# Performance work log

Measured on AMD Instinct MI355X. Metric: run time of the kernel, lower is better.

The kernel has to match this reference:

```python
import jax, jax.numpy as jnp
import numpy as np

N_HEAD = 16
SIZE_PER_HEAD = 64
NEG_BIG = 1e12


def _len_mask(lengths, T):
    # Faithful to: mask = 1 - cumsum(one_hot(len, T), 1)
    # -> 1.0 for positions < len, 0.0 for positions >= len (all ones if len == T).
    pos = jnp.arange(T)
    return (pos[None, :] < lengths[:, 0, None]).astype(jnp.float32)  # [B, T]


def setup_inputs() -> dict:
    key = jax.random.key(0)
    ks = jax.random.split(key, 8)
    B, T, D = 2, 2048, 1024
    Q_seq = jax.random.normal(ks[0], (B, T, D), dtype=jnp.float32)
    K_seq = jax.random.normal(ks[1], (B, T, D), dtype=jnp.float32)
    V_seq = jax.random.normal(ks[2], (B, T, D), dtype=jnp.float32)
    Q_len = jax.random.randint(ks[3], (B, 1), 0, T, dtype=jnp.int32)
    V_len = jax.random.randint(ks[4], (B, 1), 0, T, dtype=jnp.int32)
    s = 1.0 / np.sqrt(D)
    WQ = jax.random.normal(ks[5], (D, N_HEAD * SIZE_PER_HEAD), dtype=jnp.float32) * s
    WK = jax.random.normal(ks[6], (D, N_HEAD * SIZE_PER_HEAD), dtype=jnp.float32) * s
    WV = jax.random.normal(ks[7], (D, N_HEAD * SIZE_PER_HEAD), dtype=jnp.float32) * s
    return {"Q_seq": Q_seq, "K_seq": K_seq, "V_seq": V_seq,
            "Q_len": Q_len, "V_len": V_len, "WQ": WQ, "WK": WK, "WV": WV}


def reference(Q_seq, K_seq, V_seq, Q_len, V_len, WQ, WK, WV):
    B, Tq, _ = Q_seq.shape
    Tk = K_seq.shape[1]
    H, dh = N_HEAD, SIZE_PER_HEAD

    q = (Q_seq @ WQ).reshape(B, Tq, H, dh)  # [B,Tq,H,dh]
    k = (K_seq @ WK).reshape(B, Tk, H, dh)
    v = (V_seq @ WV).reshape(B, Tk, H, dh)

    # scaled dot-product scores [B,H,Tq,Tk]
    A = jnp.einsum('bqhd,bkhd->bhqk', q, k) / np.sqrt(dh).astype(np.float32)

    # additive key-length mask over the key axis (original: permute+mask+permute)
    kmask = _len_mask(V_len, Tk)  # [B,Tk]
    A = A - (1.0 - kmask)[:, None, None, :] * NEG_BIG
    A = jax.nn.softmax(A, axis=-1)

    O = jnp.einsum('bhqk,bkhd->bqhd', A, v).reshape(B, Tq, H * dh)

    # multiplicative query-length mask
    qmask = _len_mask(Q_len, Tq)  # [B,Tq]
    return O * qmask[:, :, None]
```

## Files before the change

### kernel.cpp

```cpp
#include <hip/hip_runtime.h>


using short8   = __attribute__((ext_vector_type(8))) short;
using floatx4  = __attribute__((ext_vector_type(4))) float;
using floatx16 = __attribute__((ext_vector_type(16))) float;
using uintx4   = __attribute__((ext_vector_type(4))) unsigned int;
using ushort4v = __attribute__((ext_vector_type(4))) unsigned short;

__device__ __forceinline__ unsigned short f2bf(float f) {
    unsigned int u = __builtin_bit_cast(unsigned int, f);
    u += 0x7fffu + ((u >> 16) & 1u);
    return (unsigned short)(u >> 16);
}

__global__ __launch_bounds__(256) void cvt_kernel(
    const float* __restrict__ Qs, const float* __restrict__ Ks,
    const float* __restrict__ Vs, const int* __restrict__ Qlen,
    const int* __restrict__ Vlen, unsigned short* __restrict__ abf)
{
    int z = blockIdx.y, row = blockIdx.x;
    int b = row >> 11, rib = row & 2047;
    int ql = Qlen[b]; int vl = Vlen[b]; int vle = vl ? vl : 2048;
    int lim = (z == 0) ? ((ql + 127) & ~127) : ((vle + 127) & ~127);
    if (rib >= lim) return;
    const float* src = (z == 0) ? Qs : ((z == 1) ? Ks : Vs);
    int t = threadIdx.x;
    float4 v = *reinterpret_cast<const float4*>(src + (size_t)row * 1024 + t * 4);
    ushort4v o;
    o[0] = f2bf(v.x); o[1] = f2bf(v.y); o[2] = f2bf(v.z); o[3] = f2bf(v.w);
    *reinterpret_cast<ushort4v*>(abf + (size_t)z * 4194304u + (size_t)row * 1024 + t * 4) = o;
}

__global__ __launch_bounds__(256) void wt_kernel(
    const float* __restrict__ W0, const float* __restrict__ W1,
    const float* __restrict__ W2, unsigned short* __restrict__ out)
{
    __shared__ float tile[64][65];
    int z = blockIdx.z;
    const float* W = (z == 0) ? W0 : ((z == 1) ? W1 : W2);
    unsigned short* O = out + (size_t)z * 1048576u;
    int r0 = blockIdx.y * 64, c0 = blockIdx.x * 64;
    int t = threadIdx.x;
#pragma unroll
    for (int i = 0; i < 16; i++) {
        int idx = t + i * 256; int r = idx >> 6, c = idx & 63;
        tile[r][c] = W[(size_t)(r0 + r) * 1024 + c0 + c];
    }
    __syncthreads();
#pragma unroll
    for (int i = 0; i < 16; i++) {
        int idx = t + i * 256; int c = idx >> 6, r = idx & 63;
        O[(size_t)(c0 + c) * 1024 + r0 + r] = f2bf(tile[r][c]);
    }
}

template <bool PRECVT>
__global__ __launch_bounds__(256) void proj_kernel(
    const float* __restrict__ Qs, const float* __restrict__ Ks,
    const float* __restrict__ Vs, const unsigned short* __restrict__ abf,
    const unsigned short* __restrict__ wt,
    const int* __restrict__ Qlen, const int* __restrict__ Vlen,
    unsigned short* __restrict__ q, unsigned short* __restrict__ k,
    unsigned short* __restrict__ vh)
{
    __shared__ alignas(16) unsigned short As[128][72];
    __shared__ alignas(16) unsigned short Bs[128][72];

    int z = blockIdx.z;
    int tid = threadIdx.x;
    int m0 = blockIdx.y * 128, n0 = blockIdx.x * 128;
    int b = m0 >> 11, rib = m0 & 2047;
    int ql = Qlen[b]; int vl = Vlen[b]; int vle = vl ? vl : 2048;
    int lim = (z == 0) ? ((ql + 127) & ~127) : ((vle + 127) & ~127);
    if (rib >= lim) return;

    const float* Af = (z == 0) ? Qs : ((z == 1) ? Ks : Vs);
    const unsigned short* Ab = abf + (size_t)z * 4194304u;
    const unsigned short* Bt = wt + (size_t)z * 1048576u;

    int w = tid >> 6, lane = tid & 63, g = lane >> 4, lr = lane & 15;
    int wr = w >> 1, wc = w & 1;

    floatx4 acc[4][4];
#pragma unroll
    for (int m = 0; m < 4; m++)
#pragma unroll
        for (int n = 0; n < 4; n++) {
#pragma unroll
            for (int r = 0; r < 4; r++) acc[m][n][r] = 0.f;
        }

    int srow = tid >> 1, scol = (tid & 1) * 32;

    short8 pa[4], pb[4];
    float4 fa[8];

    if constexpr (PRECVT) {
#pragma unroll
        for (int i = 0; i < 4; i++)
            pa[i] = *reinterpret_cast<const short8*>(Ab + (size_t)(m0 + srow) * 1024 + scol + i * 8);
    } else {
#pragma unroll
        for (int i = 0; i < 8; i++)
            fa[i] = *reinterpret_cast<const float4*>(Af + (size_t)(m0 + srow) * 1024 + scol + i * 4);
    }
#pragma unroll
    for (int i = 0; i < 4; i++)
        pb[i] = *reinterpret_cast<const short8*>(Bt + (size_t)(n0 + srow) * 1024 + scol + i * 8);

    for (int kb = 0; kb < 1024; kb += 64) {
        __syncthreads();
        if constexpr (PRECVT) {
#pragma unroll
            for (int i = 0; i < 4; i++)
                *reinterpret_cast<short8*>(&As[srow][scol + i * 8]) = pa[i];
        } else {
#pragma unroll
            for (int i = 0; i < 4; i++) {
                short8 h;
                h[0] = (short)f2bf(fa[2*i].x);   h[1] = (short)f2bf(fa[2*i].y);
                h[2] = (short)f2bf(fa[2*i].z);   h[3] = (short)f2bf(fa[2*i].w);
                h[4] = (short)f2bf(fa[2*i+1].x); h[5] = (short)f2bf(fa[2*i+1].y);
                h[6] = (short)f2bf(fa[2*i+1].z); h[7] = (short)f2bf(fa[2*i+1].w);
                *reinterpret_cast<short8*>(&As[srow][scol + i * 8]) = h;
            }
        }
#pragma unroll
        for (int i = 0; i < 4; i++)
            *reinterpret_cast<short8*>(&Bs[srow][scol + i * 8]) = pb[i];
        __syncthreads();

        if (kb + 64 < 1024) {
            if constexpr (PRECVT) {
#pragma unroll
                for (int i = 0; i < 4; i++)
                    pa[i] = *reinterpret_cast<const short8*>(Ab + (size_t)(m0 + srow) * 1024 + kb + 64 + scol + i * 8);
            } else {
#pragma unroll
                for (int i = 0; i < 8; i++)
                    fa[i] = *reinterpret_cast<const float4*>(Af + (size_t)(m0 + srow) * 1024 + kb + 64 + scol + i * 4);
            }
#pragma unroll
            for (int i = 0; i < 4; i++)
                pb[i] = *reinterpret_cast<const short8*>(Bt + (size_t)(n0 + srow) * 1024 + kb + 64 + scol + i * 8);
        }

#pragma unroll
        for (int kc = 0; kc < 2; kc++) {
            short8 af[4], bf[4];
#pragma unroll
            for (int m = 0; m < 4; m++)
                af[m] = *reinterpret_cast<const short8*>(&As[wr * 64 + m * 16 + lr][kc * 32 + g * 8]);
#pragma unroll
            for (int n = 0; n < 4; n++)
                bf[n] = *reinterpret_cast<const short8*>(&Bs[wc * 64 + n * 16 + lr][kc * 32 + g * 8]);
#pragma unroll
            for (int m = 0; m < 4; m++)
#pragma unroll
                for (int n = 0; n < 4; n++)
                    acc[m][n] = __builtin_amdgcn_mfma_f32_16x16x32_bf16(af[m], bf[n], acc[m][n], 0, 0, 0);
        }
    }

    if (z < 2) {
        unsigned short* outp = (z == 0) ? q : k;
#pragma unroll
        for (int m = 0; m < 4; m++) {
            int row0 = m0 + wr * 64 + m * 16 + g * 4;
            int tg0 = row0 & 2047;
#pragma unroll
            for (int n = 0; n < 4; n++) {
                int col = n0 + wc * 64 + n * 16 + lr;
                int hh = col >> 6, dd = col & 63;
                size_t base = ((size_t)(b * 16 + hh) * 2048 + tg0) * 64 + dd;
#pragma unroll
                for (int r = 0; r < 4; r++)
                    outp[base + (size_t)r * 64] = f2bf(acc[m][n][r]);
            }
        }
    } else {
#pragma unroll
        for (int m = 0; m < 4; m++) {
            int row0 = m0 + wr * 64 + m * 16 + g * 4;
            int tg = row0 & 2047;
#pragma unroll
            for (int n = 0; n < 4; n++) {
                int col = n0 + wc * 64 + n * 16 + lr;
                int hh = col >> 6, dd = col & 63;
                ushort4v pk;
#pragma unroll
                for (int r = 0; r < 4; r++) pk[r] = f2bf(acc[m][n][r]);
                size_t addr = ((size_t)(b * 16 + hh) * 32 + (tg >> 6)) * 4096
                            + (size_t)dd * 64 + (tg & 63);
                *reinterpret_cast<ushort4v*>(vh + addr) = pk;
            }
        }
    }
}

__global__ __launch_bounds__(128, 2) void attn_kernel(
    const unsigned short* __restrict__ q, const unsigned short* __restrict__ k,
    const unsigned short* __restrict__ vh, const int* __restrict__ Qlen,
    const int* __restrict__ Vlen, float* __restrict__ out)
{
    __shared__ float obuf[64][33];
    __shared__ float mlm[2][33];
    __shared__ float mll[2][33];

    int tid = threadIdx.x;
    int w = tid >> 6, lane = tid & 63;
    int j = lane & 31, hi = lane >> 5;

    int blk = blockIdx.x;
    int x = blk & 7, idx = blk >> 3;
    int bh = x + 8 * (idx >> 6), qtile = idx & 63;
    int b = bh >> 4, h = bh & 15;
    int qlen = Qlen[b]; int vl = Vlen[b]; int vle = vl ? vl : 2048;
    int qrow0 = qtile * 32;

    if (qrow0 >= qlen) {
        int zr = qrow0 + (tid >> 2);
        float* p = out + (size_t)(b * 2048 + zr) * 1024 + h * 64 + (tid & 3) * 16;
        float4 z4; z4.x = 0.f; z4.y = 0.f; z4.z = 0.f; z4.w = 0.f;
#pragma unroll
        for (int s = 0; s < 4; s++) *reinterpret_cast<float4*>(p + 4 * s) = z4;
        return;
    }

    int nt = (vle + 63) >> 6;
    int ntw = (nt - w + 1) >> 1;

    const unsigned short* khb = k + (size_t)(b * 16 + h) * 131072u + hi * 8;
    const unsigned short* vhb = vh + (size_t)(b * 16 + h) * 131072u + hi * 8;

    short8 kf0[4], kf1[4], vf0[4], vf1[4];
    {
        int t0 = (w < nt) ? w : (nt - 1);
        int kt = t0 << 6;
        const unsigned short* kr0 = khb + (size_t)(kt + j) * 64;
        const unsigned short* kr1 = khb + (size_t)(kt + 32 + j) * 64;
        const unsigned short* vt0 = vhb + (size_t)t0 * 4096 + j * 64;
#pragma unroll
        for (int c = 0; c < 4; c++) {
            kf0[c] = *reinterpret_cast<const short8*>(kr0 + c * 16);
            kf1[c] = *reinterpret_cast<const short8*>(kr1 + c * 16);
            vf0[c] = *reinterpret_cast<const short8*>(vt0 + c * 16);
            vf1[c] = *reinterpret_cast<const short8*>(vt0 + 2048 + c * 16);
        }
    }
    __builtin_amdgcn_sched_barrier(0);

    short8 qf[4];
    {
        const unsigned short* qp = q + (size_t)(b * 16 + h) * 131072u
                                     + (size_t)(qrow0 + j) * 64 + hi * 8;
#pragma unroll
        for (int c = 0; c < 4; c++) qf[c] = *reinterpret_cast<const short8*>(qp + c * 16);
    }

    floatx16 O0, O1;
#pragma unroll
    for (int t = 0; t < 16; t++) { O0[t] = 0.f; O1[t] = 0.f; }
    float m_r = -3.0e38f, l_r = 0.f;

    const float CEXP = 0.18033688011112042f;

    for (int m = 0; m < ntw; ++m) {
        int tix = w + 2 * m;
        int kt = tix << 6;
        int tnx = tix + 2; if (tnx >= nt) tnx = nt - 1;
        int ktn = tnx << 6;

        floatx16 s0, s1;
#pragma unroll
        for (int t = 0; t < 16; t++) { s0[t] = 0.f; s1[t] = 0.f; }
#pragma unroll
        for (int c = 0; c < 4; c++) {
            s0 = __builtin_amdgcn_mfma_f32_32x32x16_bf16(kf0[c], qf[c], s0, 0, 0, 0);
            s1 = __builtin_amdgcn_mfma_f32_32x32x16_bf16(kf1[c], qf[c], s1, 0, 0, 0);
        }

        {
            const unsigned short* kr0 = khb + (size_t)(ktn + j) * 64;
            const unsigned short* kr1 = khb + (size_t)(ktn + 32 + j) * 64;
#pragma unroll
            for (int c = 0; c < 4; c++) {
                kf0[c] = *reinterpret_cast<const short8*>(kr0 + c * 16);
                kf1[c] = *reinterpret_cast<const short8*>(kr1 + c * 16);
            }
        }
        __builtin_amdgcn_sched_barrier(0);

        if (kt + 64 > vle) {
#pragma unroll
            for (int t = 0; t < 16; t++) {
                int kl = (t & 3) + 8 * (t >> 2) + 4 * hi;
                if (kt + kl >= vle)      s0[t] = -8.0e12f;
                if (kt + 32 + kl >= vle) s1[t] = -8.0e12f;
            }
        }

        float mx = s0[0];
#pragma unroll
        for (int t = 1; t < 16; t++) mx = fmaxf(mx, s0[t]);
#pragma unroll
        for (int t = 0; t < 16; t++) mx = fmaxf(mx, s1[t]);
        float lm = fmaxf(mx, __shfl_xor(mx, 32));

        if (__any(lm > m_r + 64.f)) {
            float mn = fmaxf(m_r, lm);
            float al = __builtin_amdgcn_exp2f((m_r - mn) * CEXP);
            m_r = mn;
            l_r *= al;
#pragma unroll
            for (int t = 0; t < 16; t++) { O0[t] *= al; O1[t] *= al; }
        }
        float nm = -m_r * CEXP;
#pragma unroll
        for (int t = 0; t < 16; t++) {
            s0[t] = __builtin_amdgcn_exp2f(fmaf(s0[t], CEXP, nm));
            s1[t] = __builtin_amdgcn_exp2f(fmaf(s1[t], CEXP, nm));
        }
        float rs = 0.f;
#pragma unroll
        for (int t = 0; t < 16; t++) rs += s0[t] + s1[t];
        l_r += rs;

        unsigned int pbw[4][4];
        {
            unsigned int D[4][2];
#pragma unroll
            for (int s = 0; s < 4; s++) {
                asm("v_cvt_pk_bf16_f32 %0, %1, %2" : "=v"(D[s][0]) : "v"(s0[4*s+0]), "v"(s0[4*s+1]));
                asm("v_cvt_pk_bf16_f32 %0, %1, %2" : "=v"(D[s][1]) : "v"(s0[4*s+2]), "v"(s0[4*s+3]));
            }
#pragma unroll
            for (int u = 0; u < 2; u++) {
                asm volatile("v_permlane32_swap_b32 %0, %1" : "+v"(D[0][u]), "+v"(D[1][u]));
                asm volatile("v_permlane32_swap_b32 %0, %1" : "+v"(D[2][u]), "+v"(D[3][u]));
                pbw[0][u] = D[0][u]; pbw[0][u + 2] = D[1][u];
                pbw[1][u] = D[2][u]; pbw[1][u + 2] = D[3][u];
            }
#pragma unroll
            for (int s = 0; s < 4; s++) {
                asm("v_cvt_pk_bf16_f32 %0, %1, %2" : "=v"(D[s][0]) : "v"(s1[4*s+0]), "v"(s1[4*s+1]));
                asm("v_cvt_pk_bf16_f32 %0, %1, %2" : "=v"(D[s][1]) : "v"(s1[4*s+2]), "v"(s1[4*s+3]));
            }
#pragma unroll
            for (int u = 0; u < 2; u++) {
                asm volatile("v_permlane32_swap_b32 %0, %1" : "+v"(D[0][u]), "+v"(D[1][u]));
                asm volatile("v_permlane32_swap_b32 %0, %1" : "+v"(D[2][u]), "+v"(D[3][u]));
                pbw[2][u] = D[0][u]; pbw[2][u + 2] = D[1][u];
                pbw[3][u] = D[2][u]; pbw[3][u + 2] = D[3][u];
            }
        }

#pragma unroll
        for (int c = 0; c < 4; c++) {
            uintx4 pw; pw[0] = pbw[c][0]; pw[1] = pbw[c][1]; pw[2] = pbw[c][2]; pw[3] = pbw[c][3];
            short8 pf = __builtin_bit_cast(short8, pw);
            O0 = __builtin_amdgcn_mfma_f32_32x32x16_bf16(vf0[c], pf, O0, 0, 0, 0);
            O1 = __builtin_amdgcn_mfma_f32_32x32x16_bf16(vf1[c], pf, O1, 0, 0, 0);
        }

        {
            const unsigned short* vt = vhb + (size_t)tnx * 4096 + j * 64;
#pragma unroll
            for (int c = 0; c < 4; c++) {
                vf0[c] = *reinterpret_cast<const short8*>(vt + c * 16);
                vf1[c] = *reinterpret_cast<const short8*>(vt + 2048 + c * 16);
            }
        }
        __builtin_amdgcn_sched_barrier(0);
    }

    l_r = l_r + __shfl_xor(l_r, 32);
    if (hi == 0) mlm[w][j] = m_r;
    __syncthreads();
    float M = fmaxf(mlm[0][j], mlm[1][j]);
    float al = __builtin_amdgcn_exp2f((m_r - M) * CEXP);
#pragma unroll
    for (int t = 0; t < 16; t++) { O0[t] *= al; O1[t] *= al; }
    if (hi == 0) mll[w][j] = l_r * al;
    if (w == 1) {
#pragma unroll
        for (int t = 0; t < 16; t++) {
            obuf[lane][t]      = O0[t];
            obuf[lane][t + 16] = O1[t];
        }
    }
    __syncthreads();
    if (w == 0) {
#pragma unroll
        for (int t = 0; t < 16; t++) {
            O0[t] += obuf[lane][t];
            O1[t] += obuf[lane][t + 16];
        }
        float lt = mll[0][j] + mll[1][j];
        int qrow = qrow0 + j;
        float qm = (qrow < qlen) ? (1.0f / lt) : 0.f;
        float* ob = out + (size_t)(b * 2048 + qrow) * 1024 + h * 64;
#pragma unroll
        for (int s = 0; s < 4; s++) {
            float4 oa, obv;
            oa.x = O0[4*s+0] * qm; oa.y = O0[4*s+1] * qm; oa.z = O0[4*s+2] * qm; oa.w = O0[4*s+3] * qm;
            obv.x = O1[4*s+0] * qm; obv.y = O1[4*s+1] * qm; obv.z = O1[4*s+2] * qm; obv.w = O1[4*s+3] * qm;
            *reinterpret_cast<float4*>(ob + 8 * s + 4 * hi) = oa;
            *reinterpret_cast<float4*>(ob + 32 + 8 * s + 4 * hi) = obv;
        }
    }
}

extern "C" void kernel_launch(void* const* d_in, const int* in_sizes, int n_in,
                              void* d_out, int out_size, void* d_ws, size_t ws_size,
                              hipStream_t stream)
{
    const float* Q_seq = (const float*)d_in[0];
    const float* K_seq = (const float*)d_in[1];
    const float* V_seq = (const float*)d_in[2];
    const int*   Q_len = (const int*)d_in[3];
    const int*   V_len = (const int*)d_in[4];
    const float* WQ    = (const float*)d_in[5];
    const float* WK    = (const float*)d_in[6];
    const float* WV    = (const float*)d_in[7];
    float* outp = (float*)d_out;

    unsigned short* wsb = (unsigned short*)d_ws;
    unsigned short* wt  = wsb;
    unsigned short* qp  = wsb + (size_t)3 * 1048576u;
    unsigned short* kp  = qp + 4194304u;
    unsigned short* vhp = kp + 4194304u;
    unsigned short* abf = vhp + 4194304u;

    size_t need = ((size_t)3 * 1048576u + 3u * 4194304u + (size_t)3 * 4194304u) * 2u;
    bool precvt = ws_size >= need;

    wt_kernel<<<dim3(16, 16, 3), 256, 0, stream>>>(WQ, WK, WV, wt);
    if (precvt) {
        cvt_kernel<<<dim3(4096, 3), 256, 0, stream>>>(Q_seq, K_seq, V_seq, Q_len, V_len, abf);
        proj_kernel<true><<<dim3(8, 32, 3), 256, 0, stream>>>(
            Q_seq, K_seq, V_seq, abf, wt, Q_len, V_len, qp, kp, vhp);
    } else {
        proj_kernel<false><<<dim3(8, 32, 3), 256, 0, stream>>>(
            Q_seq, K_seq, V_seq, nullptr, wt, Q_len, V_len, qp, kp, vhp);
    }
    attn_kernel<<<dim3(2048), 128, 0, stream>>>(qp, kp, vhp, Q_len, V_len, outp);
}
```

Measured before the change: 84.30 us.

## Process two query sub-tiles per attention block and pre-swizzle Q/K/V layouts

Each attention block now handles 64 query rows as two 32-row halves that share every loaded K and V tile, halving K/V global traffic per query row and the grid size. The projection kernel writes Q, K and V in a tiled, fragment-ordered layout so each lane's short8 fragment load is contiguous. The cost is roughly doubled register use (four output accumulators and two Q fragment sets), and the launch-bounds occupancy hint is dropped, which may lower occupancy.

Result: faster. 68.01 us (-19.3%).

```diff
diff --git a/kernel.cpp b/kernel.cpp
--- a/kernel.cpp
+++ b/kernel.cpp
@@ -117,12 +117,12 @@
         } else {
 #pragma unroll
             for (int i = 0; i < 4; i++) {
-                short8 h;
-                h[0] = (short)f2bf(fa[2*i].x);   h[1] = (short)f2bf(fa[2*i].y);
-                h[2] = (short)f2bf(fa[2*i].z);   h[3] = (short)f2bf(fa[2*i].w);
-                h[4] = (short)f2bf(fa[2*i+1].x); h[5] = (short)f2bf(fa[2*i+1].y);
-                h[6] = (short)f2bf(fa[2*i+1].z); h[7] = (short)f2bf(fa[2*i+1].w);
-                *reinterpret_cast<short8*>(&As[srow][scol + i * 8]) = h;
+                short8 hcv;
+                hcv[0] = (short)f2bf(fa[2*i].x);   hcv[1] = (short)f2bf(fa[2*i].y);
+                hcv[2] = (short)f2bf(fa[2*i].z);   hcv[3] = (short)f2bf(fa[2*i].w);
+                hcv[4] = (short)f2bf(fa[2*i+1].x); hcv[5] = (short)f2bf(fa[2*i+1].y);
+                hcv[6] = (short)f2bf(fa[2*i+1].z); hcv[7] = (short)f2bf(fa[2*i+1].w);
+                *reinterpret_cast<short8*>(&As[srow][scol + i * 8]) = hcv;
             }
         }
 #pragma unroll
@@ -167,15 +167,18 @@
 #pragma unroll
         for (int m = 0; m < 4; m++) {
             int row0 = m0 + wr * 64 + m * 16 + g * 4;
-            int tg0 = row0 & 2047;
+            int tb = row0 & 2047;
+            int tile = tb >> 6, rin = tb & 63;
 #pragma unroll
             for (int n = 0; n < 4; n++) {
                 int col = n0 + wc * 64 + n * 16 + lr;
                 int hh = col >> 6, dd = col & 63;
-                size_t base = ((size_t)(b * 16 + hh) * 2048 + tg0) * 64 + dd;
+                int cc = dd >> 4, h2 = (dd >> 3) & 1, u = dd & 7;
+                size_t base = ((size_t)(b * 16 + hh) * 32 + tile) * 4096
+                            + (size_t)((cc * 2 + h2) * 512) + (size_t)rin * 8 + u;
 #pragma unroll
                 for (int r = 0; r < 4; r++)
-                    outp[base + (size_t)r * 64] = f2bf(acc[m][n][r]);
+                    outp[base + (size_t)r * 8] = f2bf(acc[m][n][r]);
             }
         }
     } else {
@@ -183,6 +186,8 @@
         for (int m = 0; m < 4; m++) {
             int row0 = m0 + wr * 64 + m * 16 + g * 4;
             int tg = row0 & 2047;
+            int tile = tg >> 6, kin = tg & 63;
+            int cc = kin >> 4, h2 = (kin >> 3) & 1, u = kin & 7;
 #pragma unroll
             for (int n = 0; n < 4; n++) {
                 int col = n0 + wc * 64 + n * 16 + lr;
@@ -190,22 +195,22 @@
                 ushort4v pk;
 #pragma unroll
                 for (int r = 0; r < 4; r++) pk[r] = f2bf(acc[m][n][r]);
-                size_t addr = ((size_t)(b * 16 + hh) * 32 + (tg >> 6)) * 4096
-                            + (size_t)dd * 64 + (tg & 63);
+                size_t addr = ((size_t)(b * 16 + hh) * 32 + tile) * 4096
+                            + (size_t)((cc * 2 + h2) * 512) + (size_t)dd * 8 + u;
                 *reinterpret_cast<ushort4v*>(vh + addr) = pk;
             }
         }
     }
 }
 
-__global__ __launch_bounds__(128, 2) void attn_kernel(
+__global__ __launch_bounds__(128) void attn_kernel(
     const unsigned short* __restrict__ q, const unsigned short* __restrict__ k,
     const unsigned short* __restrict__ vh, const int* __restrict__ Qlen,
     const int* __restrict__ Vlen, float* __restrict__ out)
 {
-    __shared__ float obuf[64][33];
-    __shared__ float mlm[2][33];
-    __shared__ float mll[2][33];
+    __shared__ float obuf[2][64][33];
+    __shared__ float mlm[2][2][33];
+    __shared__ float mll[2][2][33];
 
     int tid = threadIdx.x;
     int w = tid >> 6, lane = tid & 63;
@@ -213,84 +218,72 @@
 
     int blk = blockIdx.x;
     int x = blk & 7, idx = blk >> 3;
-    int bh = x + 8 * (idx >> 6), qtile = idx & 63;
+    int bh = x + 8 * (idx >> 5), qb = idx & 31;
     int b = bh >> 4, h = bh & 15;
     int qlen = Qlen[b]; int vl = Vlen[b]; int vle = vl ? vl : 2048;
-    int qrow0 = qtile * 32;
-
-    if (qrow0 >= qlen) {
-        int zr = qrow0 + (tid >> 2);
-        float* p = out + (size_t)(b * 2048 + zr) * 1024 + h * 64 + (tid & 3) * 16;
+
+    if (qb * 64 >= qlen) {
+        int zr = qb * 64 + (tid >> 1);
+        float* p = out + (size_t)(b * 2048 + zr) * 1024 + h * 64 + (tid & 1) * 32;
         float4 z4; z4.x = 0.f; z4.y = 0.f; z4.z = 0.f; z4.w = 0.f;
 #pragma unroll
-        for (int s = 0; s < 4; s++) *reinterpret_cast<float4*>(p + 4 * s) = z4;
+        for (int s = 0; s < 8; s++) *reinterpret_cast<float4*>(p + 4 * s) = z4;
         return;
     }
 
     int nt = (vle + 63) >> 6;
     int ntw = (nt - w + 1) >> 1;
 
-    const unsigned short* khb = k + (size_t)(b * 16 + h) * 131072u + hi * 8;
-    const unsigned short* vhb = vh + (size_t)(b * 16 + h) * 131072u + hi * 8;
+    size_t hb = (size_t)(b * 16 + h) * 131072u;
+    const unsigned short* kh = k + hb;
+    const unsigned short* vb = vh + hb;
+    int lo = hi * 512 + j * 8;
+
+    short8 qfA[4], qfB[4];
+    {
+        const unsigned short* qt = q + hb + (size_t)qb * 4096 + lo;
+#pragma unroll
+        for (int c = 0; c < 4; c++) {
+            qfA[c] = *reinterpret_cast<const short8*>(qt + c * 1024);
+            qfB[c] = *reinterpret_cast<const short8*>(qt + c * 1024 + 256);
+        }
+    }
 
     short8 kf0[4], kf1[4], vf0[4], vf1[4];
     {
         int t0 = (w < nt) ? w : (nt - 1);
-        int kt = t0 << 6;
-        const unsigned short* kr0 = khb + (size_t)(kt + j) * 64;
-        const unsigned short* kr1 = khb + (size_t)(kt + 32 + j) * 64;
-        const unsigned short* vt0 = vhb + (size_t)t0 * 4096 + j * 64;
+        const unsigned short* kt0 = kh + (size_t)t0 * 4096 + lo;
+        const unsigned short* vt0 = vb + (size_t)t0 * 4096 + lo;
 #pragma unroll
         for (int c = 0; c < 4; c++) {
-            kf0[c] = *reinterpret_cast<const short8*>(kr0 + c * 16);
-            kf1[c] = *reinterpret_cast<const short8*>(kr1 + c * 16);
-            vf0[c] = *reinterpret_cast<const short8*>(vt0 + c * 16);
-            vf1[c] = *reinterpret_cast<const short8*>(vt0 + 2048 + c * 16);
+            kf0[c] = *reinterpret_cast<const short8*>(kt0 + c * 1024);
+            kf1[c] = *reinterpret_cast<const short8*>(kt0 + c * 1024 + 256);
+            vf0[c] = *reinterpret_cast<const short8*>(vt0 + c * 1024);
+            vf1[c] = *reinterpret_cast<const short8*>(vt0 + c * 1024 + 256);
         }
     }
     __builtin_amdgcn_sched_barrier(0);
 
-    short8 qf[4];
-    {
-        const unsigned short* qp = q + (size_t)(b * 16 + h) * 131072u
-                                     + (size_t)(qrow0 + j) * 64 + hi * 8;
-#pragma unroll
-        for (int c = 0; c < 4; c++) qf[c] = *reinterpret_cast<const short8*>(qp + c * 16);
-    }
-
-    floatx16 O0, O1;
-#pragma unroll
-    for (int t = 0; t < 16; t++) { O0[t] = 0.f; O1[t] = 0.f; }
-    float m_r = -3.0e38f, l_r = 0.f;
+    floatx16 OA0, OA1, OB0, OB1;
+#pragma unroll
+    for (int t = 0; t < 16; t++) { OA0[t] = 0.f; OA1[t] = 0.f; OB0[t] = 0.f; OB1[t] = 0.f; }
+    float mA = -3.0e38f, lA = 0.f, mB = -3.0e38f, lB = 0.f;
 
     const float CEXP = 0.18033688011112042f;
 
-    for (int m = 0; m < ntw; ++m) {
-        int tix = w + 2 * m;
+    for (int mi = 0; mi < ntw; ++mi) {
+        int tix = w + 2 * mi;
         int kt = tix << 6;
         int tnx = tix + 2; if (tnx >= nt) tnx = nt - 1;
-        int ktn = tnx << 6;
 
         floatx16 s0, s1;
 #pragma unroll
         for (int t = 0; t < 16; t++) { s0[t] = 0.f; s1[t] = 0.f; }
 #pragma unroll
         for (int c = 0; c < 4; c++) {
-            s0 = __builtin_amdgcn_mfma_f32_32x32x16_bf16(kf0[c], qf[c], s0, 0, 0, 0);
-            s1 = __builtin_amdgcn_mfma_f32_32x32x16_bf16(kf1[c], qf[c], s1, 0, 0, 0);
-        }
-
-        {
-            const unsigned short* kr0 = khb + (size_t)(ktn + j) * 64;
-            const unsigned short* kr1 = khb + (size_t)(ktn + 32 + j) * 64;
-#pragma unroll
-            for (int c = 0; c < 4; c++) {
-                kf0[c] = *reinterpret_cast<const short8*>(kr0 + c * 16);
-                kf1[c] = *reinterpret_cast<const short8*>(kr1 + c * 16);
-            }
-        }
-        __builtin_amdgcn_sched_barrier(0);
-
+            s0 = __builtin_amdgcn_mfma_f32_32x32x16_bf16(kf0[c], qfA[c], s0, 0, 0, 0);
+            s1 = __builtin_amdgcn_mfma_f32_32x32x16_bf16(kf1[c], qfA[c], s1, 0, 0, 0);
+        }
         if (kt + 64 > vle) {
 #pragma unroll
             for (int t = 0; t < 16; t++) {
@@ -299,35 +292,33 @@
                 if (kt + 32 + kl >= vle) s1[t] = -8.0e12f;
             }
         }
-
-        float mx = s0[0];
-#pragma unroll
-        for (int t = 1; t < 16; t++) mx = fmaxf(mx, s0[t]);
-#pragma unroll
-        for (int t = 0; t < 16; t++) mx = fmaxf(mx, s1[t]);
-        float lm = fmaxf(mx, __shfl_xor(mx, 32));
-
-        if (__any(lm > m_r + 64.f)) {
-            float mn = fmaxf(m_r, lm);
-            float al = __builtin_amdgcn_exp2f((m_r - mn) * CEXP);
-            m_r = mn;
-            l_r *= al;
-#pragma unroll
-            for (int t = 0; t < 16; t++) { O0[t] *= al; O1[t] *= al; }
-        }
-        float nm = -m_r * CEXP;
-#pragma unroll
-        for (int t = 0; t < 16; t++) {
-            s0[t] = __builtin_amdgcn_exp2f(fmaf(s0[t], CEXP, nm));
-            s1[t] = __builtin_amdgcn_exp2f(fmaf(s1[t], CEXP, nm));
-        }
-        float rs = 0.f;
-#pragma unroll
-        for (int t = 0; t < 16; t++) rs += s0[t] + s1[t];
-        l_r += rs;
-
-        unsigned int pbw[4][4];
         {
+            float mx = s0[0];
+#pragma unroll
+            for (int t = 1; t < 16; t++) mx = fmaxf(mx, s0[t]);
+#pragma unroll
+            for (int t = 0; t < 16; t++) mx = fmaxf(mx, s1[t]);
+            float lm = fmaxf(mx, __shfl_xor(mx, 32));
+            if (__any(lm > mA + 64.f)) {
+                float mn = fmaxf(mA, lm);
+                float al = __builtin_amdgcn_exp2f((mA - mn) * CEXP);
+                mA = mn; lA *= al;
+#pragma unroll
+                for (int t = 0; t < 16; t++) { OA0[t] *= al; OA1[t] *= al; }
+            }
+            float nm = -mA * CEXP;
+#pragma unroll
+            for (int t = 0; t < 16; t++) {
+                s0[t] = __builtin_amdgcn_exp2f(fmaf(s0[t], CEXP, nm));
+                s1[t] = __builtin_amdgcn_exp2f(fmaf(s1[t], CEXP, nm));
+            }
+            float rs = 0.f;
+#pragma unroll
+            for (int t = 0; t < 16; t++) rs += s0[t] + s1[t];
+            lA += rs;
+        }
+        {
+            unsigned int pbw[4][4];
             unsigned int D[4][2];
 #pragma unroll
             for (int s = 0; s < 4; s++) {
@@ -353,60 +344,158 @@
                 pbw[2][u] = D[0][u]; pbw[2][u + 2] = D[1][u];
                 pbw[3][u] = D[2][u]; pbw[3][u + 2] = D[3][u];
             }
-        }
-
+#pragma unroll
+            for (int c = 0; c < 4; c++) {
+                uintx4 pw; pw[0] = pbw[c][0]; pw[1] = pbw[c][1]; pw[2] = pbw[c][2]; pw[3] = pbw[c][3];
+                short8 pf = __builtin_bit_cast(short8, pw);
+                OA0 = __builtin_amdgcn_mfma_f32_32x32x16_bf16(vf0[c], pf, OA0, 0, 0, 0);
+                OA1 = __builtin_amdgcn_mfma_f32_32x32x16_bf16(vf1[c], pf, OA1, 0, 0, 0);
+            }
+        }
+
+#pragma unroll
+        for (int t = 0; t < 16; t++) { s0[t] = 0.f; s1[t] = 0.f; }
 #pragma unroll
         for (int c = 0; c < 4; c++) {
-            uintx4 pw; pw[0] = pbw[c][0]; pw[1] = pbw[c][1]; pw[2] = pbw[c][2]; pw[3] = pbw[c][3];
-            short8 pf = __builtin_bit_cast(short8, pw);
-            O0 = __builtin_amdgcn_mfma_f32_32x32x16_bf16(vf0[c], pf, O0, 0, 0, 0);
-            O1 = __builtin_amdgcn_mfma_f32_32x32x16_bf16(vf1[c], pf, O1, 0, 0, 0);
-        }
-
+            s0 = __builtin_amdgcn_mfma_f32_32x32x16_bf16(kf0[c], qfB[c], s0, 0, 0, 0);
+            s1 = __builtin_amdgcn_mfma_f32_32x32x16_bf16(kf1[c], qfB[c], s1, 0, 0, 0);
+        }
         {
-            const unsigned short* vt = vhb + (size_t)tnx * 4096 + j * 64;
+            const unsigned short* kn = kh + (size_t)tnx * 4096 + lo;
 #pragma unroll
             for (int c = 0; c < 4; c++) {
-                vf0[c] = *reinterpret_cast<const short8*>(vt + c * 16);
-                vf1[c] = *reinterpret_cast<const short8*>(vt + 2048 + c * 16);
+                kf0[c] = *reinterpret_cast<const short8*>(kn + c * 1024);
+                kf1[c] = *reinterpret_cast<const short8*>(kn + c * 1024 + 256);
             }
         }
         __builtin_amdgcn_sched_barrier(0);
-    }
-
-    l_r = l_r + __shfl_xor(l_r, 32);
-    if (hi == 0) mlm[w][j] = m_r;
+
+        if (kt + 64 > vle) {
+#pragma unroll
+            for (int t = 0; t < 16; t++) {
+                int kl = (t & 3) + 8 * (t >> 2) + 4 * hi;
+                if (kt + kl >= vle)      s0[t] = -8.0e12f;
+                if (kt + 32 + kl >= vle) s1[t] = -8.0e12f;
+            }
+        }
+        {
+            float mx = s0[0];
+#pragma unroll
+            for (int t = 1; t < 16; t++) mx = fmaxf(mx, s0[t]);
+#pragma unroll
+            for (int t = 0; t < 16; t++) mx = fmaxf(mx, s1[t]);
+            float lm = fmaxf(mx, __shfl_xor(mx, 32));
+            if (__any(lm > mB + 64.f)) {
+                float mn = fmaxf(mB, lm);
+                float al = __builtin_amdgcn_exp2f((mB - mn) * CEXP);
+                mB = mn; lB *= al;
+#pragma unroll
+                for (int t = 0; t < 16; t++) { OB0[t] *= al; OB1[t] *= al; }
+            }
+            float nm = -mB * CEXP;
+#pragma unroll
+            for (int t = 0; t < 16; t++) {
+                s0[t] = __builtin_amdgcn_exp2f(fmaf(s0[t], CEXP, nm));
+                s1[t] = __builtin_amdgcn_exp2f(fmaf(s1[t], CEXP, nm));
+            }
+            float rs = 0.f;
+#pragma unroll
+            for (int t = 0; t < 16; t++) rs += s0[t] + s1[t];
+            lB += rs;
+        }
+        {
+            unsigned int pbw[4][4];
+            unsigned int D[4][2];
+#pragma unroll
+            for (int s = 0; s < 4; s++) {
+                asm("v_cvt_pk_bf16_f32 %0, %1, %2" : "=v"(D[s][0]) : "v"(s0[4*s+0]), "v"(s0[4*s+1]));
+                asm("v_cvt_pk_bf16_f32 %0, %1, %2" : "=v"(D[s][1]) : "v"(s0[4*s+2]), "v"(s0[4*s+3]));
+            }
+#pragma unroll
+            for (int u = 0; u < 2; u++) {
+                asm volatile("v_permlane32_swap_b32 %0, %1" : "+v"(D[0][u]), "+v"(D[1][u]));
+                asm volatile("v_permlane32_swap_b32 %0, %1" : "+v"(D[2][u]), "+v"(D[3][u]));
+                pbw[0][u] = D[0][u]; pbw[0][u + 2] = D[1][u];
+                pbw[1][u] = D[2][u]; pbw[1][u + 2] = D[3][u];
+            }
+#pragma unroll
+            for (int s = 0; s < 4; s++) {
+                asm("v_cvt_pk_bf16_f32 %0, %1, %2" : "=v"(D[s][0]) : "v"(s1[4*s+0]), "v"(s1[4*s+1]));
+                asm("v_cvt_pk_bf16_f32 %0, %1, %2" : "=v"(D[s][1]) : "v"(s1[4*s+2]), "v"(s1[4*s+3]));
+            }
+#pragma unroll
+            for (int u = 0; u < 2; u++) {
+                asm volatile("v_permlane32_swap_b32 %0, %1" : "+v"(D[0][u]), "+v"(D[1][u]));
+                asm volatile("v_permlane32_swap_b32 %0, %1" : "+v"(D[2][u]), "+v"(D[3][u]));
+                pbw[2][u] = D[0][u]; pbw[2][u + 2] = D[1][u];
+                pbw[3][u] = D[2][u]; pbw[3][u + 2] = D[3][u];
+            }
+#pragma unroll
+            for (int c = 0; c < 4; c++) {
+                uintx4 pw; pw[0] = pbw[c][0]; pw[1] = pbw[c][1]; pw[2] = pbw[c][2]; pw[3] = pbw[c][3];
+                short8 pf = __builtin_bit_cast(short8, pw);
+                OB0 = __builtin_amdgcn_mfma_f32_32x32x16_bf16(vf0[c], pf, OB0, 0, 0, 0);
+                OB1 = __builtin_amdgcn_mfma_f32_32x32x16_bf16(vf1[c], pf, OB1, 0, 0, 0);
+            }
+        }
+        {
+            const unsigned short* vn = vb + (size_t)tnx * 4096 + lo;
+#pragma unroll
+            for (int c = 0; c < 4; c++) {
+                vf0[c] = *reinterpret_cast<const short8*>(vn + c * 1024);
+                vf1[c] = *reinterpret_cast<const short8*>(vn + c * 1024 + 256);
+            }
+        }
+        __builtin_amdgcn_sched_barrier(0);
+    }
+
+    lA = lA + __shfl_xor(lA, 32);
+    lB = lB + __shfl_xor(lB, 32);
+    if (hi == 0) { mlm[0][w][j] = mA; mlm[1][w][j] = mB; }
     __syncthreads();
-    float M = fmaxf(mlm[0][j], mlm[1][j]);
-    float al = __builtin_amdgcn_exp2f((m_r - M) * CEXP);
-#pragma unroll
-    for (int t = 0; t < 16; t++) { O0[t] *= al; O1[t] *= al; }
-    if (hi == 0) mll[w][j] = l_r * al;
+    float MA = fmaxf(mlm[0][0][j], mlm[0][1][j]);
+    float MB = fmaxf(mlm[1][0][j], mlm[1][1][j]);
+    float alA = __builtin_amdgcn_exp2f((mA - MA) * CEXP);
+    float alB = __builtin_amdgcn_exp2f((mB - MB) * CEXP);
+#pragma unroll
+    for (int t = 0; t < 16; t++) { OA0[t] *= alA; OA1[t] *= alA; OB0[t] *= alB; OB1[t] *= alB; }
+    if (hi == 0) { mll[0][w][j] = lA * alA; mll[1][w][j] = lB * alB; }
     if (w == 1) {
 #pragma unroll
         for (int t = 0; t < 16; t++) {
-            obuf[lane][t]      = O0[t];
-            obuf[lane][t + 16] = O1[t];
+            obuf[0][lane][t]      = OA0[t];
+            obuf[0][lane][t + 16] = OA1[t];
+            obuf[1][lane][t]      = OB0[t];
+            obuf[1][lane][t + 16] = OB1[t];
         }
     }
     __syncthreads();
     if (w == 0) {
 #pragma unroll
         for (int t = 0; t < 16; t++) {
-            O0[t] += obuf[lane][t];
-            O1[t] += obuf[lane][t + 16];
-        }
-        float lt = mll[0][j] + mll[1][j];
-        int qrow = qrow0 + j;
-        float qm = (qrow < qlen) ? (1.0f / lt) : 0.f;
-        float* ob = out + (size_t)(b * 2048 + qrow) * 1024 + h * 64;
+            OA0[t] += obuf[0][lane][t];
+            OA1[t] += obuf[0][lane][t + 16];
+            OB0[t] += obuf[1][lane][t];
+            OB1[t] += obuf[1][lane][t + 16];
+        }
+        float ltA = mll[0][0][j] + mll[0][1][j];
+        float ltB = mll[1][0][j] + mll[1][1][j];
+        int qrA = qb * 64 + j, qrB = qb * 64 + 32 + j;
+        float qmA = (qrA < qlen) ? (1.0f / ltA) : 0.f;
+        float qmB = (qrB < qlen) ? (1.0f / ltB) : 0.f;
+        float* oa = out + (size_t)(b * 2048 + qrA) * 1024 + h * 64;
+        float* ob = out + (size_t)(b * 2048 + qrB) * 1024 + h * 64;
 #pragma unroll
         for (int s = 0; s < 4; s++) {
-            float4 oa, obv;
-            oa.x = O0[4*s+0] * qm; oa.y = O0[4*s+1] * qm; oa.z = O0[4*s+2] * qm; oa.w = O0[4*s+3] * qm;
-            obv.x = O1[4*s+0] * qm; obv.y = O1[4*s+1] * qm; obv.z = O1[4*s+2] * qm; obv.w = O1[4*s+3] * qm;
-            *reinterpret_cast<float4*>(ob + 8 * s + 4 * hi) = oa;
-            *reinterpret_cast<float4*>(ob + 32 + 8 * s + 4 * hi) = obv;
+            float4 v0, v1;
+            v0.x = OA0[4*s+0] * qmA; v0.y = OA0[4*s+1] * qmA; v0.z = OA0[4*s+2] * qmA; v0.w = OA0[4*s+3] * qmA;
+            v1.x = OA1[4*s+0] * qmA; v1.y = OA1[4*s+1] * qmA; v1.z = OA1[4*s+2] * qmA; v1.w = OA1[4*s+3] * qmA;
+            *reinterpret_cast<float4*>(oa + 8 * s + 4 * hi) = v0;
+            *reinterpret_cast<float4*>(oa + 32 + 8 * s + 4 * hi) = v1;
+            v0.x = OB0[4*s+0] * qmB; v0.y = OB0[4*s+1] * qmB; v0.z = OB0[4*s+2] * qmB; v0.w = OB0[4*s+3] * qmB;
+            v1.x = OB1[4*s+0] * qmB; v1.y = OB1[4*s+1] * qmB; v1.z = OB1[4*s+2] * qmB; v1.w = OB1[4*s+3] * qmB;
+            *reinterpret_cast<float4*>(ob + 8 * s + 4 * hi) = v0;
+            *reinterpret_cast<float4*>(ob + 32 + 8 * s + 4 * hi) = v1;
         }
     }
 }
@@ -444,5 +533,5 @@
         proj_kernel<false><<<dim3(8, 32, 3), 256, 0, stream>>>(
             Q_seq, K_seq, V_seq, nullptr, wt, Q_len, V_len, qp, kp, vhp);
     }
-    attn_kernel<<<dim3(2048), 128, 0, stream>>>(qp, kp, vhp, Q_len, V_len, outp);
+    attn_kernel<<<dim3(1024), 128, 0, stream>>>(qp, kp, vhp, Q_len, V_len, outp);
 }
```
